# Performance work log

Measured on AMD Instinct MI355X. Metric: run time of the kernel, lower is better.

The kernel has to match this reference:

```python
import jax, jax.numpy as jnp
import numpy as np

T = 15
L = 10.0
LAM = 0.1
RHO = 1.0
NUM_CONV_A = 32
NUM_CONV_B = 32
DICT_DIM = 7
STRIDE_A = 1
STRIDE_B = 1
DN = ('NCHW', 'OIHW', 'NCHW')


def _fro_normalize(W):
    # normalize each (d, d) filter slice by its Frobenius norm (torch F.normalize, p='fro', dim=(-1,-2))
    n = jnp.sqrt(jnp.sum(W * W, axis=(-1, -2), keepdims=True))
    return W / jnp.maximum(n, 1e-12)


def _conv(y, W, s):
    # torch F.conv2d(y, W, stride=s), VALID padding
    return jax.lax.conv_general_dilated(y, W, (s, s), 'VALID', dimension_numbers=DN)


def _convT(x, W, s):
    # torch F.conv_transpose2d(x, W, stride=s); W in forward-conv layout (O, I, kh, kw)
    return jax.lax.conv_transpose(x, W, (s, s), 'VALID', dimension_numbers=DN, transpose_kernel=True)


def setup_inputs() -> dict:
    key = jax.random.key(0)
    ky, ka, kb = jax.random.split(key, 3)
    y = jax.random.normal(ky, (16, 1, 256, 256), dtype=jnp.float32)
    A = _fro_normalize(jax.random.normal(ka, (NUM_CONV_A, 1, DICT_DIM, DICT_DIM), dtype=jnp.float32))
    B = _fro_normalize(jax.random.normal(kb, (NUM_CONV_B, 1, DICT_DIM, DICT_DIM), dtype=jnp.float32))
    return {'y': y, 'A': A, 'B': B}


def reference(y, A, B):
    n, _, H, W = y.shape
    Dx = (H - DICT_DIM) // STRIDE_A + 1
    Du = (H - DICT_DIM) // STRIDE_B + 1
    Dx2 = (W - DICT_DIM) // STRIDE_A + 1
    Du2 = (W - DICT_DIM) // STRIDE_B + 1
    x0 = jnp.zeros((n, NUM_CONV_A, Dx, Dx2), dtype=y.dtype)
    u0 = jnp.zeros((n, NUM_CONV_B, Du, Du2), dtype=y.dtype)

    def step(carry, _):
        x_old, x_tmp, u_old, u_tmp, t_old = carry
        Ax = _convT((1.0 + 1.0 / RHO) * x_tmp, A, STRIDE_A)
        Bu = _convT(u_tmp, B, STRIDE_B)
        res = y - (Ax + Bu)
        x_new = x_tmp + _conv(res, A, STRIDE_A) / L
        u_new = u_tmp + _conv(res, B, STRIDE_B) / L
        # twosided soft-threshold
        u_new = jax.nn.relu(jnp.abs(u_new) - LAM / L) * jnp.sign(u_new)
        t_new = (1.0 + jnp.sqrt(1.0 + 4.0 * t_old * t_old)) / 2.0
        c = (t_old - 1.0) / t_new
        x_tmp2 = x_new + c * (x_new - x_old)
        u_tmp2 = u_new + c * (u_new - u_old)
        return (x_new, x_tmp2, u_new, u_tmp2, t_new), None

    init = (x0, x0, u0, u0, jnp.float32(1.0))
    (x_new, _, u_new, _, _), _ = jax.lax.scan(step, init, None, length=T)

    Ax_hat = _convT(x_new, A, STRIDE_A)
    Bu_hat = _convT(u_new, B, STRIDE_B)
    y_hat = Ax_hat + Bu_hat
    return y_hat, x_new, u_new, Ax_hat, Bu_hat
```

## Files before the change

kernel.cpp:

```cpp
#include <hip/hip_runtime.h>
#include <cmath>

#define NB 16
#define CC 32
#define HH 256
#define WW 256
#define DD 250
#define ALPHA 2.0f
#define INVL 0.1f
#define THR 0.01f

#define IMG_SZ (HH*WW)
#define IMG_TOT (NB*IMG_SZ)
#define FLD_SZ (DD*DD)
#define FLD_TOT ((size_t)NB*CC*FLD_SZ)

#define SRS 264

__device__ __forceinline__ float rfl(float x) {
    return __int_as_float(__builtin_amdgcn_readfirstlane(__float_as_int(x)));
}
__device__ __forceinline__ float sthr(float v) {
    float a = fabsf(v) - THR; a = a > 0.f ? a : 0.f;
    return (v > 0.f) ? a : ((v < 0.f) ? -a : 0.f);
}

#define CONV_ROW(ACC, Aa) do { \
    _Pragma("unroll") \
    for (int b = 0; b < 7; ++b) { \
        const float wv = wt[Aa][b]; \
        ACC.x += wv*win[b+0]; ACC.y += wv*win[b+1]; \
        ACC.z += wv*win[b+2]; ACC.w += wv*win[b+3]; \
    } } while (0)

#define GATH_ROW(ACC, Aa) do { \
    _Pragma("unroll") \
    for (int b = 0; b < 7; ++b) { \
        const float wv = wt[Aa][b]; \
        ACC.x += wv*win[8-b+0]; ACC.y += wv*win[8-b+1]; \
        ACC.z += wv*win[8-b+2]; ACC.w += wv*win[8-b+3]; \
    } } while (0)

__global__ __launch_bounds__(512, 4) void k_step(
    const float* __restrict__ rin,
    const float* sx_cur, const float* su_cur,
    float* sx_on, float* su_on,
    float* __restrict__ Ximg, float* __restrict__ Uimg,
    const float* __restrict__ Afil, const float* __restrict__ Bfil,
    float cmom, int first)
{
    __shared__ __align__(16) float resT[22*SRS];
    __shared__ __align__(16) float stile[16*SRS];

    const int p0  = blockIdx.x * 16;
    const int f   = blockIdx.y;
    const int n   = blockIdx.z;
    const int tid = threadIdx.x;
    const bool isx = (f == 0);

    {
        float4 z = make_float4(0.f,0.f,0.f,0.f);
        float4* sp = (float4*)&stile[0];
        for (int i = tid; i < 16*SRS/4; i += 512) sp[i] = z;
    }
    {
        const float* rb = rin + (size_t)n * IMG_SZ;
        for (int i = tid; i < 22*66; i += 512) {
            int r  = i / 66;
            int c4 = (i - r*66) << 2;
            int gr = p0 + r;
            float4 v = make_float4(0.f,0.f,0.f,0.f);
            if (gr < HH && c4 < WW) v = *(const float4*)(rb + gr*WW + c4);
            *(float4*)&resT[r*SRS + c4] = v;
        }
    }
    __syncthreads();

    const int rg  = tid >> 6;
    const int q4  = (tid & 63) << 2;
    const bool qok = (q4 <= 248);
    const int p_0 = p0 + 2*rg;

    const float* Wb   = isx ? Afil : Bfil;
    const float* scur = isx ? sx_cur : su_cur;
    float*       sON  = isx ? sx_on  : su_on;
    float*       img  = (isx ? Ximg : Uimg) + (size_t)n * IMG_SZ;

    const bool momentum = (!first) && (cmom != 0.f);
    const bool plain    = (!first) && (cmom == 0.f);

    float4 ia0 = make_float4(0.f,0.f,0.f,0.f), ia1 = ia0, ia2 = ia0;

    const size_t fbase = (size_t)n * CC * FLD_SZ;
    const bool r0ok = qok && (p_0     < DD);
    const bool r1ok = qok && (p_0 + 1 < DD);
    const size_t off0 = fbase + (size_t)p_0*DD + q4;
    const size_t off1 = off0 + DD;

    for (int c = 0; c < CC; ++c) {
        float wt[7][7];
        {
            const float* Wp = Wb + c*49;
#pragma unroll
            for (int a = 0; a < 7; ++a)
#pragma unroll
                for (int b = 0; b < 7; ++b)
                    wt[a][b] = rfl(Wp[a*7 + b]);
        }

        const size_t co = (size_t)c * FLD_SZ;
        float4 sc0 = make_float4(0.f,0.f,0.f,0.f), sc1 = sc0, so0 = sc0, so1 = sc0;
        if (momentum) {
            if (r0ok) { sc0 = *(const float4*)(scur + co + off0);
                        so0 = *(const float4*)(sON  + co + off0); }
            if (r1ok) { sc1 = *(const float4*)(scur + co + off1);
                        so1 = *(const float4*)(sON  + co + off1); }
        } else if (plain) {
            if (r0ok) sc0 = *(const float4*)(scur + co + off0);
            if (r1ok) sc1 = *(const float4*)(scur + co + off1);
        }

        float4 a0 = make_float4(0.f,0.f,0.f,0.f), a1 = a0;
#pragma unroll
        for (int rr = 0; rr < 8; ++rr) {
            const float* lp = &resT[(2*rg + rr)*SRS + q4];
            float4 A0 = *(const float4*)lp;
            float4 A1 = *(const float4*)(lp + 4);
            float4 A2 = *(const float4*)(lp + 8);
            const float win[12] = {A0.x,A0.y,A0.z,A0.w, A1.x,A1.y,A1.z,A1.w,
                                   A2.x,A2.y,A2.z,A2.w};
            if (rr <= 6) CONV_ROW(a0, rr);
            if (rr >= 1) CONV_ROW(a1, rr-1);
        }

        float4 o0 = make_float4(a0.x*INVL, a0.y*INVL, a0.z*INVL, a0.w*INVL);
        float4 o1 = make_float4(a1.x*INVL, a1.y*INVL, a1.z*INVL, a1.w*INVL);
        if (momentum) {
            o0.x += sc0.x + cmom*(sc0.x - so0.x);
            o0.y += sc0.y + cmom*(sc0.y - so0.y);
            o0.z += sc0.z + cmom*(sc0.z - so0.z);
            o0.w += sc0.w + cmom*(sc0.w - so0.w);
            o1.x += sc1.x + cmom*(sc1.x - so1.x);
            o1.y += sc1.y + cmom*(sc1.y - so1.y);
            o1.z += sc1.z + cmom*(sc1.z - so1.z);
            o1.w += sc1.w + cmom*(sc1.w - so1.w);
        } else if (plain) {
            o0.x += sc0.x; o0.y += sc0.y; o0.z += sc0.z; o0.w += sc0.w;
            o1.x += sc1.x; o1.y += sc1.y; o1.z += sc1.z; o1.w += sc1.w;
        }
        if (!isx) {
            o0.x = sthr(o0.x); o0.y = sthr(o0.y); o0.z = sthr(o0.z); o0.w = sthr(o0.w);
            o1.x = sthr(o1.x); o1.y = sthr(o1.y); o1.z = sthr(o1.z); o1.w = sthr(o1.w);
        }

        if (r0ok) {
            float* dst = sON + co + off0;
            if (q4 <= 244) *(float4*)dst = o0;
            else           *(float2*)dst = make_float2(o0.x, o0.y);
        }
        if (r1ok) {
            float* dst = sON + co + off1;
            if (q4 <= 244) *(float4*)dst = o1;
            else           *(float2*)dst = make_float2(o1.x, o1.y);
        }

        __syncthreads();

        if (r0ok) {
            float* d0 = &stile[(2*rg)*SRS + q4 + 8];
            if (q4 <= 244) *(float4*)d0 = o0;
            else           *(float2*)d0 = make_float2(o0.x, o0.y);
        }
        if (r1ok) {
            float* d1 = &stile[(2*rg + 1)*SRS + q4 + 8];
            if (q4 <= 244) *(float4*)d1 = o1;
            else           *(float2*)d1 = make_float2(o1.x, o1.y);
        }
        __syncthreads();

#pragma unroll
        for (int k9 = 0; k9 < 9; ++k9) {
            const int k = 3*rg - 6 + k9;
            if (k >= 0 && k < 16) {
                const float* sp = &stile[k*SRS + q4];
                float4 B0 = *(const float4*)sp;
                float4 B1 = *(const float4*)(sp + 4);
                float4 B2 = *(const float4*)(sp + 8);
                const float win[12] = {B0.x,B0.y,B0.z,B0.w, B1.x,B1.y,B1.z,B1.w,
                                       B2.x,B2.y,B2.z,B2.w};
                if (k9 <= 6)            GATH_ROW(ia0, 6 - k9);
                if (k9 >= 1 && k9 <= 7) GATH_ROW(ia1, 7 - k9);
                if (k9 >= 2)            GATH_ROW(ia2, 8 - k9);
            }
        }
    }

#pragma unroll
    for (int d = 0; d < 3; ++d) {
        const int h = 3*rg + d;
        if (h < 22) {
            const int habs = p0 + h;
            if (habs < HH) {
                float4 v = (d == 0) ? ia0 : (d == 1) ? ia1 : ia2;
                float* ip = img + (size_t)habs*WW + q4;
                if (h >= 6 && h <= 15) {
                    *(float4*)ip = v;
                } else {
                    atomicAdd(ip + 0, v.x);
                    atomicAdd(ip + 1, v.y);
                    atomicAdd(ip + 2, v.z);
                    atomicAdd(ip + 3, v.w);
                }
            }
        }
    }
}

__global__ __launch_bounds__(256) void k_res(
    const float* __restrict__ y,
    float* Xp, float* Up,
    float* Xc, float* Uc,
    float* __restrict__ resb, float cm)
{
    int i = blockIdx.x*256 + threadIdx.x;
    if (i >= IMG_TOT/4) return;
    float4 xc = ((const float4*)Xp)[i];
    float4 uc = ((const float4*)Up)[i];
    float4 xo = make_float4(0.f,0.f,0.f,0.f), uo = xo;
    if (cm != 0.f) {
        xo = ((const float4*)Xc)[i];
        uo = ((const float4*)Uc)[i];
    }
    ((float4*)Xc)[i] = xc;
    ((float4*)Uc)[i] = uc;
    float4 z = make_float4(0.f,0.f,0.f,0.f);
    ((float4*)Xp)[i] = z;
    ((float4*)Up)[i] = z;
    float4 yv = ((const float4*)y)[i];
    const float cp = 1.f + cm;
    float4 r;
    r.x = yv.x - ALPHA*(cp*xc.x - cm*xo.x) - (cp*uc.x - cm*uo.x);
    r.y = yv.y - ALPHA*(cp*xc.y - cm*xo.y) - (cp*uc.y - cm*uo.y);
    r.z = yv.z - ALPHA*(cp*xc.z - cm*xo.z) - (cp*uc.z - cm*uo.z);
    r.w = yv.w - ALPHA*(cp*xc.w - cm*xo.w) - (cp*uc.w - cm*uo.w);
    ((float4*)resb)[i] = r;
}

__global__ __launch_bounds__(256) void k_zero2(float* a, float* b)
{
    int i = blockIdx.x*256 + threadIdx.x;
    if (i < IMG_TOT/4) {
        float4 z = make_float4(0.f,0.f,0.f,0.f);
        ((float4*)a)[i] = z;
        ((float4*)b)[i] = z;
    }
}

__global__ __launch_bounds__(256) void k_final(
    const float* __restrict__ axh, const float* __restrict__ buh,
    float* __restrict__ yhat)
{
    int i = blockIdx.x*256 + threadIdx.x;
    if (i < IMG_TOT/4) {
        float4 x = ((const float4*)axh)[i];
        float4 u = ((const float4*)buh)[i];
        float4 s;
        s.x = x.x + u.x; s.y = x.y + u.y; s.z = x.z + u.z; s.w = x.w + u.w;
        ((float4*)yhat)[i] = s;
    }
}

extern "C" void kernel_launch(void* const* d_in, const int* in_sizes, int n_in,
                              void* d_out, int out_size, void* d_ws, size_t ws_size,
                              hipStream_t stream) {
    const float* y = (const float*)d_in[0];
    const float* A = (const float*)d_in[1];
    const float* B = (const float*)d_in[2];

    float* out  = (float*)d_out;
    float* yhat = out;
    float* xout = out + IMG_TOT;
    float* uout = xout + FLD_TOT;
    float* axh  = uout + FLD_TOT;
    float* buh  = axh + IMG_TOT;

    float* ws   = (float*)d_ws;
    float* Px0  = ws;
    float* Pu0  = Px0 + FLD_TOT;
    float* Xc   = Pu0 + FLD_TOT;
    float* Uc   = Xc + IMG_TOT;

    float* Px[2] = {Px0, xout};
    float* Pu[2] = {Pu0, uout};
    float* res   = yhat;

    float cv[15];
    {
        float t = 1.0f;
        for (int k = 0; k < 15; ++k) {
            float tn = (1.0f + sqrtf(1.0f + 4.0f*t*t)) * 0.5f;
            cv[k] = (t - 1.0f) / tn;
            t = tn;
        }
    }

    dim3 blk512(512), blk256(256);
    dim3 gS(16, 2, NB);
    int  gE = (IMG_TOT/4 + 255)/256;

    k_zero2<<<gE, blk256, 0, stream>>>(axh, buh);

    k_step<<<gS, blk512, 0, stream>>>(y, Px[0], Pu[0], Px[1], Pu[1],
                                      axh, buh, A, B, 0.0f, 1);

    for (int t = 1; t < 15; ++t) {
        float cm = cv[t-1];
        k_res<<<gE, blk256, 0, stream>>>(y, axh, buh, Xc, Uc, res, cm);
        k_step<<<gS, blk512, 0, stream>>>(res, Px[t&1], Pu[t&1],
                                          Px[(t+1)&1], Pu[(t+1)&1],
                                          axh, buh, A, B, cm, 0);
    }

    k_final<<<gE, blk256, 0, stream>>>(axh, buh, yhat);
}
```

Baseline: 3.816 ms.

## Split channel loop across two block halves with separate partial image buffers

New measurement: 4.151 ms. 8.8% more time.

```diff
diff --git a/kernel.cpp b/kernel.cpp
--- a/kernel.cpp
+++ b/kernel.cpp
@@ -45,17 +45,21 @@
     const float* __restrict__ rin,
     const float* sx_cur, const float* su_cur,
     float* sx_on, float* su_on,
-    float* __restrict__ Ximg, float* __restrict__ Uimg,
+    float* __restrict__ Xp0, float* __restrict__ Xp1,
+    float* __restrict__ Up0, float* __restrict__ Up1,
     const float* __restrict__ Afil, const float* __restrict__ Bfil,
-    float cmom, int first)
+    float cmom, int first, int nhalf, int nch)
 {
     __shared__ __align__(16) float resT[22*SRS];
     __shared__ __align__(16) float stile[16*SRS];
 
-    const int p0  = blockIdx.x * 16;
-    const int f   = blockIdx.y;
-    const int n   = blockIdx.z;
-    const int tid = threadIdx.x;
+    const int p0   = blockIdx.x * 16;
+    const int role = blockIdx.y;
+    const int f    = role / nhalf;
+    const int half = role - f*nhalf;
+    const int ch0  = half * nch;
+    const int n    = blockIdx.z;
+    const int tid  = threadIdx.x;
     const bool isx = (f == 0);
 
     {
@@ -84,7 +88,8 @@
     const float* Wb   = isx ? Afil : Bfil;
     const float* scur = isx ? sx_cur : su_cur;
     float*       sON  = isx ? sx_on  : su_on;
-    float*       img  = (isx ? Ximg : Uimg) + (size_t)n * IMG_SZ;
+    float*       img  = (isx ? (half ? Xp1 : Xp0) : (half ? Up1 : Up0))
+                        + (size_t)n * IMG_SZ;
 
     const bool momentum = (!first) && (cmom != 0.f);
     const bool plain    = (!first) && (cmom == 0.f);
@@ -97,7 +102,8 @@
     const size_t off0 = fbase + (size_t)p_0*DD + q4;
     const size_t off1 = off0 + DD;
 
-    for (int c = 0; c < CC; ++c) {
+    for (int ci = 0; ci < nch; ++ci) {
+        const int c = ch0 + ci;
         float wt[7][7];
         {
             const float* Wp = Wb + c*49;
@@ -218,24 +224,28 @@
 
 __global__ __launch_bounds__(256) void k_res(
     const float* __restrict__ y,
-    float* Xp, float* Up,
+    float* Xp0, float* Xp1, float* Up0, float* Up1,
     float* Xc, float* Uc,
-    float* __restrict__ resb, float cm)
+    float* __restrict__ resb, float cm, int nparts)
 {
     int i = blockIdx.x*256 + threadIdx.x;
     if (i >= IMG_TOT/4) return;
-    float4 xc = ((const float4*)Xp)[i];
-    float4 uc = ((const float4*)Up)[i];
-    float4 xo = make_float4(0.f,0.f,0.f,0.f), uo = xo;
+    float4 z = make_float4(0.f,0.f,0.f,0.f);
+    float4 xc = ((const float4*)Xp0)[i];  ((float4*)Xp0)[i] = z;
+    float4 uc = ((const float4*)Up0)[i];  ((float4*)Up0)[i] = z;
+    if (nparts == 2) {
+        float4 t = ((const float4*)Xp1)[i];  ((float4*)Xp1)[i] = z;
+        xc.x += t.x; xc.y += t.y; xc.z += t.z; xc.w += t.w;
+        float4 s = ((const float4*)Up1)[i];  ((float4*)Up1)[i] = z;
+        uc.x += s.x; uc.y += s.y; uc.z += s.z; uc.w += s.w;
+    }
+    float4 xo = z, uo = z;
     if (cm != 0.f) {
         xo = ((const float4*)Xc)[i];
         uo = ((const float4*)Uc)[i];
     }
     ((float4*)Xc)[i] = xc;
     ((float4*)Uc)[i] = uc;
-    float4 z = make_float4(0.f,0.f,0.f,0.f);
-    ((float4*)Xp)[i] = z;
-    ((float4*)Up)[i] = z;
     float4 yv = ((const float4*)y)[i];
     const float cp = 1.f + cm;
     float4 r;
@@ -246,28 +256,37 @@
     ((float4*)resb)[i] = r;
 }
 
-__global__ __launch_bounds__(256) void k_zero2(float* a, float* b)
+__global__ __launch_bounds__(256) void k_zero4(float* a, float* b, float* c, float* d)
 {
     int i = blockIdx.x*256 + threadIdx.x;
     if (i < IMG_TOT/4) {
         float4 z = make_float4(0.f,0.f,0.f,0.f);
         ((float4*)a)[i] = z;
         ((float4*)b)[i] = z;
+        ((float4*)c)[i] = z;
+        ((float4*)d)[i] = z;
     }
 }
 
 __global__ __launch_bounds__(256) void k_final(
-    const float* __restrict__ axh, const float* __restrict__ buh,
-    float* __restrict__ yhat)
+    float* axh, const float* __restrict__ Xp1,
+    float* buh, const float* __restrict__ Up1,
+    float* __restrict__ yhat, int nparts)
 {
     int i = blockIdx.x*256 + threadIdx.x;
-    if (i < IMG_TOT/4) {
-        float4 x = ((const float4*)axh)[i];
-        float4 u = ((const float4*)buh)[i];
-        float4 s;
-        s.x = x.x + u.x; s.y = x.y + u.y; s.z = x.z + u.z; s.w = x.w + u.w;
-        ((float4*)yhat)[i] = s;
-    }
+    if (i >= IMG_TOT/4) return;
+    float4 x = ((const float4*)axh)[i];
+    float4 u = ((const float4*)buh)[i];
+    if (nparts == 2) {
+        float4 t = ((const float4*)Xp1)[i];
+        x.x += t.x; x.y += t.y; x.z += t.z; x.w += t.w;
+        float4 s = ((const float4*)Up1)[i];
+        u.x += s.x; u.y += s.y; u.z += s.z; u.w += s.w;
+    }
+    ((float4*)axh)[i] = x;
+    ((float4*)buh)[i] = u;
+    float4 s2 = make_float4(x.x+u.x, x.y+u.y, x.z+u.z, x.w+u.w);
+    ((float4*)yhat)[i] = s2;
 }
 
 extern "C" void kernel_launch(void* const* d_in, const int* in_sizes, int n_in,
@@ -289,6 +308,13 @@
     float* Pu0  = Px0 + FLD_TOT;
     float* Xc   = Pu0 + FLD_TOT;
     float* Uc   = Xc + IMG_TOT;
+    float* Xp1  = Uc + IMG_TOT;
+    float* Up1  = Xp1 + IMG_TOT;
+
+    size_t need2 = (2*FLD_TOT + 4*(size_t)IMG_TOT) * sizeof(float);
+    const int nhalf = (ws_size >= need2) ? 2 : 1;
+    const int nch   = CC / nhalf;
+    if (nhalf == 1) { Xp1 = axh; Up1 = buh; }
 
     float* Px[2] = {Px0, xout};
     float* Pu[2] = {Pu0, uout};
@@ -305,21 +331,24 @@
     }
 
     dim3 blk512(512), blk256(256);
-    dim3 gS(16, 2, NB);
+    dim3 gS(16, 2*nhalf, NB);
     int  gE = (IMG_TOT/4 + 255)/256;
 
-    k_zero2<<<gE, blk256, 0, stream>>>(axh, buh);
+    k_zero4<<<gE, blk256, 0, stream>>>(axh, buh, Xp1, Up1);
 
     k_step<<<gS, blk512, 0, stream>>>(y, Px[0], Pu[0], Px[1], Pu[1],
-                                      axh, buh, A, B, 0.0f, 1);
+                                      axh, Xp1, buh, Up1, A, B, 0.0f, 1,
+                                      nhalf, nch);
 
     for (int t = 1; t < 15; ++t) {
         float cm = cv[t-1];
-        k_res<<<gE, blk256, 0, stream>>>(y, axh, buh, Xc, Uc, res, cm);
+        k_res<<<gE, blk256, 0, stream>>>(y, axh, Xp1, buh, Up1, Xc, Uc,
+                                         res, cm, nhalf);
         k_step<<<gS, blk512, 0, stream>>>(res, Px[t&1], Pu[t&1],
                                           Px[(t+1)&1], Pu[(t+1)&1],
-                                          axh, buh, A, B, cm, 0);
-    }
-
-    k_final<<<gE, blk256, 0, stream>>>(axh, buh, yhat);
-}
+                                          axh, Xp1, buh, Up1, A, B, cm, 0,
+                                          nhalf, nch);
+    }
+
+    k_final<<<gE, blk256, 0, stream>>>(axh, Xp1, buh, Up1, yhat, nhalf);
+}
```
